# Optimization experiments

Hardware: AMD Instinct MI355X
Metric: run time of the kernel (lower is better)

The kernel has to match this reference:

```python
import jax, jax.numpy as jnp
import numpy as np

N_NODES = 100_000
N_EDGES = 1_200_000


def _lap_weights(src, dst, attr, n):
    # PyG get_laplacian(sym) + ChebConv scaling with lambda_max=2.0:
    # L_hat = (2/lmax)(I - D^-1/2 A D^-1/2) - I = -D^-1/2 A D^-1/2 (zero diagonal)
    deg = jnp.zeros((n,), attr.dtype).at[src].add(attr)
    dis = jnp.where(deg > 0, jax.lax.rsqrt(jnp.maximum(deg, 1e-30)), 0.0)
    return -(dis[src] * attr * dis[dst])


def _prop(x, src, dst, lw, n):
    # y_i = sum_{(j->i)} lw_e * x_j   (gather -> scale -> scatter-add)
    return jnp.zeros((n, x.shape[1]), x.dtype).at[dst].add(lw[:, None] * x[src])


def _cheb(x, src, dst, lw, W, b):
    # W: [K, F_in, F_out]; Tx0 = x, Tx1 = L_hat x (K<=2 here)
    out = x @ W[0]
    if W.shape[0] > 1:
        tx1 = _prop(x, src, dst, lw, x.shape[0])
        out = out + tx1 @ W[1]
    return out + b


def setup_inputs() -> dict:
    key = jax.random.key(0)
    ks = jax.random.split(key, 11)
    x = jax.random.normal(ks[0], (N_NODES, 20), jnp.float32)
    edge_index = jax.random.randint(ks[1], (2, N_EDGES), 0, N_NODES, jnp.int32)
    attr = jax.random.uniform(ks[2], (N_EDGES,), jnp.float32)
    def glorot(k, shape):
        fan = shape[-2] + shape[-1]
        return jax.random.normal(k, shape, jnp.float32) * jnp.sqrt(2.0 / fan)
    return {
        "x": x, "edge_index": edge_index, "attr": attr,
        "w1": glorot(ks[3], (1, 20, 32)), "b1": jnp.zeros((32,), jnp.float32),
        "w2": glorot(ks[4], (2, 32, 64)), "b2": jnp.zeros((64,), jnp.float32),
        "w3": glorot(ks[5], (2, 64, 2)), "b3": jnp.zeros((2,), jnp.float32),
        "gate_w": glorot(ks[6], (2, 1)), "gate_b": jnp.zeros((1,), jnp.float32),
    }


def reference(x, edge_index, attr, w1, b1, w2, b2, w3, b3, gate_w, gate_b):
    n = x.shape[0]
    src, dst = edge_index[0], edge_index[1]
    lw = _lap_weights(src, dst, attr, n)
    h = jax.nn.leaky_relu(_cheb(x, src, dst, lw, w1, b1))   # [N, 32]
    h = jax.nn.leaky_relu(_cheb(h, src, dst, lw, w2, b2))   # [N, 64]
    h = _cheb(h, src, dst, lw, w3, b3)                       # [N, 2]
    # GlobalAttention with batch = zeros (single graph): softmax over nodes
    gate = jax.nn.softmax(h @ gate_w + gate_b, axis=0)       # [N, 1]
    pooled = jnp.sum(gate * h, axis=0, keepdims=True)        # [1, 2]
    return jax.nn.log_softmax(pooled, axis=1)
```

## Files before the change

### kernel.cpp

```cpp
#include <hip/hip_runtime.h>
#include <hip/hip_bf16.h>
#include <math.h>

#define N_NODES 100000
#define N_EDGES 1200000
#define E4 (N_EDGES / 4)
#define G2B ((N_NODES + 255) / 256)
#define NB_L1 G2B
#define RANGE 12800
#define NRANGE 8
#define CHK 32
#define NB_DEG (NRANGE * CHK)
#define GPC ((E4 + CHK - 1) / CHK)
#define NBIN 391
#define BINCAP 3584
#define NB_P1 256
#define GP1 ((E4 + NB_P1 - 1) / NB_P1)
#define WQ (8.f * 32767.f)

__device__ __forceinline__ float disf(float d) {
    return (d > 0.f) ? rsqrtf(d) : 0.f;
}

__global__ void degbin_kernel(const int4* __restrict__ src4, const float4* __restrict__ attr4,
                              float* __restrict__ partial) {
    __shared__ float ldeg[RANGE];
    int rb = blockIdx.x;
    int r = rb / CHK;
    int c = rb - r * CHK;
    int base = r * RANGE;
    for (int j = threadIdx.x; j < RANGE; j += blockDim.x) ldeg[j] = 0.f;
    __syncthreads();
    int g0 = c * GPC;
    int g1 = g0 + GPC; if (g1 > E4) g1 = E4;
    for (int g = g0 + threadIdx.x; g < g1; g += blockDim.x) {
        int4 s = src4[g];
        float4 a = attr4[g];
        unsigned o;
        o = (unsigned)(s.x - base); if (o < RANGE) atomicAdd(&ldeg[o], a.x);
        o = (unsigned)(s.y - base); if (o < RANGE) atomicAdd(&ldeg[o], a.y);
        o = (unsigned)(s.z - base); if (o < RANGE) atomicAdd(&ldeg[o], a.z);
        o = (unsigned)(s.w - base); if (o < RANGE) atomicAdd(&ldeg[o], a.w);
    }
    __syncthreads();
    float* dstp = partial + (size_t)rb * RANGE;
    for (int j = threadIdx.x; j < RANGE; j += blockDim.x) dstp[j] = ldeg[j];
}

__global__ void degred_kernel(const float* __restrict__ partial, float* __restrict__ deg) {
    int i = blockIdx.x * blockDim.x + threadIdx.x;
    if (i >= N_NODES) return;
    int r = i / RANGE;
    int j = i - r * RANGE;
    const float* p = partial + (size_t)r * CHK * RANGE + j;
    float s = 0.f;
#pragma unroll
    for (int c = 0; c < CHK; c++) s += p[(size_t)c * RANGE];
    deg[i] = s;
}

__global__ void p1l1_kernel(const int4* __restrict__ src4, const int4* __restrict__ dst4,
                            const float4* __restrict__ attr4, const float* __restrict__ deg,
                            const float* __restrict__ x, const float* __restrict__ w1,
                            const float* __restrict__ b1,
                            int* __restrict__ binCursor, uint2* __restrict__ binRegion,
                            signed char* __restrict__ h1q, float* __restrict__ sscale) {
    __shared__ int lhist[NBIN];
    __shared__ int lbase[NBIN];
    __shared__ int lcnt[NBIN];
    __shared__ float sw[20 * 32];
    __shared__ float sb[32];

    if (blockIdx.x < NB_P1) {
        int g0 = blockIdx.x * GP1;
        int g1 = g0 + GP1; if (g1 > E4) g1 = E4;
        for (int j = threadIdx.x; j < NBIN; j += blockDim.x) { lhist[j] = 0; lcnt[j] = 0; }
        __syncthreads();
        for (int g = g0 + threadIdx.x; g < g1; g += blockDim.x) {
            int4 d = dst4[g];
            atomicAdd(&lhist[d.x >> 8], 1);
            atomicAdd(&lhist[d.y >> 8], 1);
            atomicAdd(&lhist[d.z >> 8], 1);
            atomicAdd(&lhist[d.w >> 8], 1);
        }
        __syncthreads();
        for (int j = threadIdx.x; j < NBIN; j += blockDim.x)
            lbase[j] = (lhist[j] > 0) ? atomicAdd(&binCursor[j], lhist[j]) : 0;
        __syncthreads();
        for (int g = g0 + threadIdx.x; g < g1; g += blockDim.x) {
            int4 s = src4[g];
            int4 d = dst4[g];
            float4 a = attr4[g];
            {
                int bin = d.x >> 8;
                float w = a.x * disf(deg[s.x]);
                int pos = lbase[bin] + atomicAdd(&lcnt[bin], 1);
                if (pos < BINCAP)
                    binRegion[(size_t)bin * BINCAP + pos] =
                        make_uint2(((unsigned)s.x << 8) | (unsigned)(d.x & 255), __float_as_uint(w));
            }
            {
                int bin = d.y >> 8;
                float w = a.y * disf(deg[s.y]);
                int pos = lbase[bin] + atomicAdd(&lcnt[bin], 1);
                if (pos < BINCAP)
                    binRegion[(size_t)bin * BINCAP + pos] =
                        make_uint2(((unsigned)s.y << 8) | (unsigned)(d.y & 255), __float_as_uint(w));
            }
            {
                int bin = d.z >> 8;
                float w = a.z * disf(deg[s.z]);
                int pos = lbase[bin] + atomicAdd(&lcnt[bin], 1);
                if (pos < BINCAP)
                    binRegion[(size_t)bin * BINCAP + pos] =
                        make_uint2(((unsigned)s.z << 8) | (unsigned)(d.z & 255), __float_as_uint(w));
            }
            {
                int bin = d.w >> 8;
                float w = a.w * disf(deg[s.w]);
                int pos = lbase[bin] + atomicAdd(&lcnt[bin], 1);
                if (pos < BINCAP)
                    binRegion[(size_t)bin * BINCAP + pos] =
                        make_uint2(((unsigned)s.w << 8) | (unsigned)(d.w & 255), __float_as_uint(w));
            }
        }
    } else {
        for (int t = threadIdx.x; t < 20 * 32; t += blockDim.x) sw[t] = w1[t];
        if (threadIdx.x < 32) sb[threadIdx.x] = b1[threadIdx.x];
        __syncthreads();
        int i = (blockIdx.x - NB_P1) * blockDim.x + threadIdx.x;
        if (i >= N_NODES) return;
        float xr[20];
#pragma unroll
        for (int k = 0; k < 20; k++) xr[k] = x[(size_t)i * 20 + k];
        float row[32];
        float rmax = 0.f;
#pragma unroll
        for (int j = 0; j < 32; j++) {
            float a = sb[j];
#pragma unroll
            for (int k = 0; k < 20; k++) a += xr[k] * sw[k * 32 + j];
            a = (a > 0.f) ? a : 0.01f * a;
            row[j] = a;
            rmax = fmaxf(rmax, fabsf(a));
        }
        float sc = fmaxf(rmax * (1.f / 127.f), 1e-4f);
        float inv = 1.f / sc;
        sscale[i] = sc;
#pragma unroll
        for (int j = 0; j < 32; j++) {
            h1q[(size_t)i * 32 + j] = (signed char)lrintf(row[j] * inv);
        }
    }
}

__global__ void binscan_kernel(const int* __restrict__ binCursor, int* __restrict__ bin_start) {
    __shared__ int sm[512];
    int t = threadIdx.x;
    int v = 0;
    if (t < NBIN) {
        v = binCursor[t];
        if (v > BINCAP) v = BINCAP;
    }
    sm[t] = v;
    __syncthreads();
    for (int off = 1; off < 512; off <<= 1) {
        int u = (t >= off) ? sm[t - off] : 0;
        __syncthreads();
        sm[t] += u;
        __syncthreads();
    }
    if (t < NBIN) bin_start[t + 1] = sm[t];
    if (t == 0) bin_start[0] = 0;
}

__global__ void p2_kernel(const uint2* __restrict__ binRegion, const int* __restrict__ bin_start,
                          const float* __restrict__ sscale,
                          int* __restrict__ row_start, unsigned* __restrict__ csr) {
    __shared__ uint2 recs[BINCAP];
    __shared__ int hist[256];
    __shared__ int excl[256];
    __shared__ int cnt[256];
    int b = blockIdx.x;
    int t = threadIdx.x;
    int base = bin_start[b];
    int c = bin_start[b + 1] - base;
    const uint2* reg = binRegion + (size_t)b * BINCAP;
    for (int j = t; j < c; j += 256) recs[j] = reg[j];
    hist[t] = 0; cnt[t] = 0;
    __syncthreads();
    for (int j = t; j < c; j += 256) atomicAdd(&hist[recs[j].x & 255u], 1);
    __syncthreads();
    int v = hist[t];
    excl[t] = v;
    __syncthreads();
    for (int off = 1; off < 256; off <<= 1) {
        int u = (t >= off) ? excl[t - off] : 0;
        __syncthreads();
        excl[t] += u;
        __syncthreads();
    }
    int ex = excl[t] - v;
    row_start[b * 256 + t] = base + ex;
    if (b == NBIN - 1 && t == 255) row_start[NBIN * 256] = bin_start[NBIN];
    __syncthreads();
    hist[t] = ex;
    __syncthreads();
    for (int j = t; j < c; j += 256) {
        unsigned w0 = recs[j].x;
        int low = (int)(w0 & 255u);
        int src = (int)(w0 >> 8);
        float w = __uint_as_float(recs[j].y);
        float ws = w * sscale[src] * WQ;
        unsigned q = (unsigned)(ws + 0.5f);
        if (q > 32767u) q = 32767u;
        int pos = hist[low] + atomicAdd(&cnt[low], 1);
        csr[base + pos] = ((unsigned)src << 15) | q;
    }
}

__global__ void gl2_kernel(const int* __restrict__ row_start, const unsigned* __restrict__ csr,
                           const float* __restrict__ deg, const signed char* __restrict__ h1q,
                           const float* __restrict__ sscale,
                           const float* __restrict__ w2, const float* __restrict__ b2,
                           const float* __restrict__ w3,
                           float2* __restrict__ z0, float2* __restrict__ z1w) {
    __shared__ float s0[32 * 64];
    __shared__ float s1[32 * 64];
    __shared__ float sw3[256];
    __shared__ float sb[64];
    __shared__ float h1s[8][32];
    __shared__ float t1s[8][32];
    for (int t = threadIdx.x; t < 32 * 64; t += blockDim.x) {
        s0[t] = w2[t];
        s1[t] = w2[32 * 64 + t];
    }
    for (int t = threadIdx.x; t < 256; t += blockDim.x) sw3[t] = w3[t];
    if (threadIdx.x < 64) sb[threadIdx.x] = b2[threadIdx.x];
    __syncthreads();

    int grp = threadIdx.x >> 5;
    int lane = threadIdx.x & 31;
    int e4 = lane >> 3;
    int fg = lane & 7;
    int node = blockIdx.x * 8 + grp;
    bool alive = (node < N_NODES);

    int acc0 = 0, acc1 = 0, acc2 = 0, acc3 = 0;
    if (alive) {
        int rs = row_start[node], re = row_start[node + 1];
        for (int j = rs + e4; j < re; j += 4) {
            unsigned e = csr[j];
            int sa = (int)(e >> 15);
            int wq = (int)(e & 0x7FFFu);
            int packed = *reinterpret_cast<const int*>(h1q + (size_t)sa * 32 + fg * 4);
            acc0 += wq * (int)(signed char)(packed);
            acc1 += wq * (int)(signed char)(packed >> 8);
            acc2 += wq * (int)(signed char)(packed >> 16);
            acc3 += wq * (int)(signed char)(packed >> 24);
        }
    }
    acc0 += __shfl_xor(acc0, 8);  acc0 += __shfl_xor(acc0, 16);
    acc1 += __shfl_xor(acc1, 8);  acc1 += __shfl_xor(acc1, 16);
    acc2 += __shfl_xor(acc2, 8);  acc2 += __shfl_xor(acc2, 16);
    acc3 += __shfl_xor(acc3, 8);  acc3 += __shfl_xor(acc3, 16);

    if (alive && e4 == 0) {
        float dn = -disf(deg[node]) * (1.f / WQ);
        int packed = *reinterpret_cast<const int*>(h1q + (size_t)node * 32 + fg * 4);
        float sc = sscale[node];
        h1s[grp][fg * 4 + 0] = sc * (float)(signed char)(packed);
        h1s[grp][fg * 4 + 1] = sc * (float)(signed char)(packed >> 8);
        h1s[grp][fg * 4 + 2] = sc * (float)(signed char)(packed >> 16);
        h1s[grp][fg * 4 + 3] = sc * (float)(signed char)(packed >> 24);
        t1s[grp][fg * 4 + 0] = dn * (float)acc0;
        t1s[grp][fg * 4 + 1] = dn * (float)acc1;
        t1s[grp][fg * 4 + 2] = dn * (float)acc2;
        t1s[grp][fg * 4 + 3] = dn * (float)acc3;
    }
    __syncthreads();

    int f = lane;
    float a0 = sb[f], a1 = sb[f + 32];
#pragma unroll 8
    for (int k = 0; k < 32; k++) {
        float h = h1s[grp][k];
        float tv = t1s[grp][k];
        a0 += h * s0[k * 64 + f]      + tv * s1[k * 64 + f];
        a1 += h * s0[k * 64 + f + 32] + tv * s1[k * 64 + f + 32];
    }
    float v0 = (a0 > 0.f) ? a0 : 0.01f * a0;
    float v1 = (a1 > 0.f) ? a1 : 0.01f * a1;

    float z00 = v0 * sw3[f * 2 + 0] + v1 * sw3[(f + 32) * 2 + 0];
    float z01 = v0 * sw3[f * 2 + 1] + v1 * sw3[(f + 32) * 2 + 1];
    float z10 = v0 * sw3[128 + f * 2 + 0] + v1 * sw3[128 + (f + 32) * 2 + 0];
    float z11 = v0 * sw3[128 + f * 2 + 1] + v1 * sw3[128 + (f + 32) * 2 + 1];
#pragma unroll
    for (int m = 16; m > 0; m >>= 1) {
        z00 += __shfl_xor(z00, m);
        z01 += __shfl_xor(z01, m);
        z10 += __shfl_xor(z10, m);
        z11 += __shfl_xor(z11, m);
    }
    if (alive && f == 0) {
        z0[node] = make_float2(z00, z01);
        float isc = 1.f / sscale[node];
        z1w[node] = make_float2(z10 * isc, z11 * isc);
    }
}

__global__ void g2acc_kernel(const int* __restrict__ row_start, const unsigned* __restrict__ csr,
                             const float* __restrict__ deg,
                             const float2* __restrict__ z0, const float2* __restrict__ z1w,
                             const float* __restrict__ b3, const float* __restrict__ gw,
                             const float* __restrict__ gb, float4* __restrict__ quads) {
    __shared__ float sm[256], ss[256], s0[256], s1[256];
    int t = threadIdx.x;
    int i = blockIdx.x * blockDim.x + t;
    float m = -INFINITY, se = 0.f, a0 = 0.f, a1 = 0.f;
    if (i < N_NODES) {
        int rs = row_start[i], re = row_start[i + 1];
        float acc0 = 0.f, acc1 = 0.f;
        for (int j = rs; j < re; j++) {
            unsigned e = csr[j];
            int s = (int)(e >> 15);
            float wq = (float)(e & 0x7FFFu);
            float2 zv = z1w[s];
            acc0 += wq * zv.x;
            acc1 += wq * zv.y;
        }
        float di = -disf(deg[i]) * (1.f / WQ);
        float2 z0v = z0[i];
        float o0 = z0v.x + di * acc0 + b3[0];
        float o1 = z0v.y + di * acc1 + b3[1];
        m = o0 * gw[0] + o1 * gw[1] + gb[0];
        se = 1.f; a0 = o0; a1 = o1;
    }
    sm[t] = m; ss[t] = se; s0[t] = a0; s1[t] = a1;
    __syncthreads();
    for (int s = 128; s > 0; s >>= 1) {
        if (t < s) {
            float mb = sm[t + s];
            if (mb != -INFINITY) {
                float ma = sm[t];
                if (ma == -INFINITY) {
                    sm[t] = mb; ss[t] = ss[t + s]; s0[t] = s0[t + s]; s1[t] = s1[t + s];
                } else if (mb <= ma) {
                    float c = __expf(mb - ma);
                    ss[t] += ss[t + s] * c;
                    s0[t] += s0[t + s] * c;
                    s1[t] += s1[t + s] * c;
                } else {
                    float c = __expf(ma - mb);
                    ss[t] = ss[t] * c + ss[t + s];
                    s0[t] = s0[t] * c + s0[t + s];
                    s1[t] = s1[t] * c + s1[t + s];
                    sm[t] = mb;
                }
            }
        }
        __syncthreads();
    }
    if (t == 0) quads[blockIdx.x] = make_float4(sm[0], ss[0], s0[0], s1[0]);
}

__global__ void accB_kernel(const float4* __restrict__ quads, float* __restrict__ out) {
    __shared__ float sm[512], ss[512], s0[512], s1[512];
    int t = threadIdx.x;
    float m = -INFINITY, se = 0.f, a0 = 0.f, a1 = 0.f;
    if (t < G2B) {
        float4 q = quads[t];
        m = q.x; se = q.y; a0 = q.z; a1 = q.w;
    }
    sm[t] = m; ss[t] = se; s0[t] = a0; s1[t] = a1;
    __syncthreads();
    for (int s = 256; s > 0; s >>= 1) {
        if (t < s) {
            float mb = sm[t + s];
            if (mb != -INFINITY) {
                float ma = sm[t];
                if (ma == -INFINITY) {
                    sm[t] = mb; ss[t] = ss[t + s]; s0[t] = s0[t + s]; s1[t] = s1[t + s];
                } else if (mb <= ma) {
                    float c = __expf(mb - ma);
                    ss[t] += ss[t + s] * c;
                    s0[t] += s0[t + s] * c;
                    s1[t] += s1[t + s] * c;
                } else {
                    float c = __expf(ma - mb);
                    ss[t] = ss[t] * c + ss[t + s];
                    s0[t] = s0[t] * c + s0[t + s];
                    s1[t] = s1[t] * c + s1[t + s];
                    sm[t] = mb;
                }
            }
        }
        __syncthreads();
    }
    if (t == 0) {
        float se0 = ss[0];
        float p0 = s0[0] / se0;
        float p1 = s1[0] / se0;
        float mm = fmaxf(p0, p1);
        float l = mm + logf(__expf(p0 - mm) + __expf(p1 - mm));
        out[0] = p0 - l;
        out[1] = p1 - l;
    }
}

extern "C" void kernel_launch(void* const* d_in, const int* in_sizes, int n_in,
                              void* d_out, int out_size, void* d_ws, size_t ws_size,
                              hipStream_t stream) {
    const float* x    = (const float*)d_in[0];
    const int*   ei   = (const int*)d_in[1];
    const float* attr = (const float*)d_in[2];
    const float* w1   = (const float*)d_in[3];
    const float* b1   = (const float*)d_in[4];
    const float* w2   = (const float*)d_in[5];
    const float* b2   = (const float*)d_in[6];
    const float* w3   = (const float*)d_in[7];
    const float* b3   = (const float*)d_in[8];
    const float* gw   = (const float*)d_in[9];
    const float* gb   = (const float*)d_in[10];
    float* out = (float*)d_out;

    const int4*   src4  = (const int4*)ei;
    const int4*   dst4  = (const int4*)(ei + N_EDGES);
    const float4* attr4 = (const float4*)attr;

    float* ws = (float*)d_ws;
    size_t off = 0;
    int*      binCursor = (int*)(ws + off); off += NBIN;
    int*      bin_start = (int*)(ws + off); off += NBIN + 1;
    float*    deg       = ws + off; off += N_NODES;
    float*    sscale    = ws + off; off += N_NODES;
    int*      row_start = (int*)(ws + off); off += NBIN * 256 + 1;
    float*    partial   = ws + off; off += (size_t)NB_DEG * RANGE;
    off = (off + 3) & ~(size_t)3;
    uint2*    binRegion = (uint2*)(ws + off); off += (size_t)NBIN * BINCAP * 2;
    unsigned* csr       = (unsigned*)(ws + off); off += N_EDGES;
    signed char* h1q    = (signed char*)(ws + off); off += (size_t)N_NODES * 8;
    float2*   z0  = (float2*)(ws + off); off += (size_t)N_NODES * 2;
    float2*   z1w = (float2*)(ws + off); off += (size_t)N_NODES * 2;
    off = (off + 3) & ~(size_t)3;
    float4*   quads = (float4*)(ws + off); off += (size_t)G2B * 4;

    const int B = 256;
    auto cdiv = [](long long a, long long b) { return (int)((a + b - 1) / b); };

    hipMemsetAsync(binCursor, 0, NBIN * sizeof(int), stream);

    degbin_kernel<<<NB_DEG, B, 0, stream>>>(src4, attr4, partial);
    degred_kernel<<<cdiv(N_NODES, B), B, 0, stream>>>(partial, deg);

    p1l1_kernel<<<NB_P1 + NB_L1, B, 0, stream>>>(src4, dst4, attr4, deg, x, w1, b1,
                                                 binCursor, binRegion, h1q, sscale);

    binscan_kernel<<<1, 512, 0, stream>>>(binCursor, bin_start);

    p2_kernel<<<NBIN, B, 0, stream>>>(binRegion, bin_start, sscale, row_start, csr);

    gl2_kernel<<<cdiv(N_NODES, 8), B, 0, stream>>>(row_start, csr, deg, h1q, sscale,
                                                   w2, b2, w3, z0, z1w);

    g2acc_kernel<<<G2B, B, 0, stream>>>(row_start, csr, deg, z0, z1w, b3, gw, gb, quads);

    accB_kernel<<<1, 512, 0, stream>>>(quads, out);
}
```

Before: 162.4 us.

## Restructure gl2 to one 64-lane wave per node and amortize weight loads

Result: slower. 244.3 us (+50.4%).

```diff
diff --git a/kernel.cpp b/kernel.cpp
--- a/kernel.cpp
+++ b/kernel.cpp
@@ -9,14 +9,16 @@
 #define NB_L1 G2B
 #define RANGE 12800
 #define NRANGE 8
-#define CHK 32
+#define CHK 64
 #define NB_DEG (NRANGE * CHK)
 #define GPC ((E4 + CHK - 1) / CHK)
 #define NBIN 391
 #define BINCAP 3584
-#define NB_P1 256
+#define NB_P1 512
 #define GP1 ((E4 + NB_P1 - 1) / NB_P1)
 #define WQ (8.f * 32767.f)
+#define GL2_NPB 64
+#define NB_GL2 ((N_NODES + GL2_NPB - 1) / GL2_NPB)
 
 __device__ __forceinline__ float disf(float d) {
     return (d > 0.f) ? rsqrtf(d) : 0.f;
@@ -229,84 +231,88 @@
     __shared__ float s1[32 * 64];
     __shared__ float sw3[256];
     __shared__ float sb[64];
-    __shared__ float h1s[8][32];
-    __shared__ float t1s[8][32];
-    for (int t = threadIdx.x; t < 32 * 64; t += blockDim.x) {
-        s0[t] = w2[t];
-        s1[t] = w2[32 * 64 + t];
-    }
-    for (int t = threadIdx.x; t < 256; t += blockDim.x) sw3[t] = w3[t];
-    if (threadIdx.x < 64) sb[threadIdx.x] = b2[threadIdx.x];
-    __syncthreads();
-
-    int grp = threadIdx.x >> 5;
-    int lane = threadIdx.x & 31;
-    int e4 = lane >> 3;
+    int tid = threadIdx.x;
+    for (int t = tid; t < 32 * 64; t += 512) { s0[t] = w2[t]; s1[t] = w2[2048 + t]; }
+    for (int t = tid; t < 256; t += 512) sw3[t] = w3[t];
+    if (tid < 64) sb[tid] = b2[tid];
+    __syncthreads();
+
+    int wave = tid >> 6;
+    int lane = tid & 63;
     int fg = lane & 7;
-    int node = blockIdx.x * 8 + grp;
-    bool alive = (node < N_NODES);
-
-    int acc0 = 0, acc1 = 0, acc2 = 0, acc3 = 0;
-    if (alive) {
-        int rs = row_start[node], re = row_start[node + 1];
-        for (int j = rs + e4; j < re; j += 4) {
-            unsigned e = csr[j];
-            int sa = (int)(e >> 15);
-            int wq = (int)(e & 0x7FFFu);
-            int packed = *reinterpret_cast<const int*>(h1q + (size_t)sa * 32 + fg * 4);
-            acc0 += wq * (int)(signed char)(packed);
-            acc1 += wq * (int)(signed char)(packed >> 8);
-            acc2 += wq * (int)(signed char)(packed >> 16);
-            acc3 += wq * (int)(signed char)(packed >> 24);
-        }
-    }
-    acc0 += __shfl_xor(acc0, 8);  acc0 += __shfl_xor(acc0, 16);
-    acc1 += __shfl_xor(acc1, 8);  acc1 += __shfl_xor(acc1, 16);
-    acc2 += __shfl_xor(acc2, 8);  acc2 += __shfl_xor(acc2, 16);
-    acc3 += __shfl_xor(acc3, 8);  acc3 += __shfl_xor(acc3, 16);
-
-    if (alive && e4 == 0) {
-        float dn = -disf(deg[node]) * (1.f / WQ);
-        int packed = *reinterpret_cast<const int*>(h1q + (size_t)node * 32 + fg * 4);
-        float sc = sscale[node];
-        h1s[grp][fg * 4 + 0] = sc * (float)(signed char)(packed);
-        h1s[grp][fg * 4 + 1] = sc * (float)(signed char)(packed >> 8);
-        h1s[grp][fg * 4 + 2] = sc * (float)(signed char)(packed >> 16);
-        h1s[grp][fg * 4 + 3] = sc * (float)(signed char)(packed >> 24);
-        t1s[grp][fg * 4 + 0] = dn * (float)acc0;
-        t1s[grp][fg * 4 + 1] = dn * (float)acc1;
-        t1s[grp][fg * 4 + 2] = dn * (float)acc2;
-        t1s[grp][fg * 4 + 3] = dn * (float)acc3;
-    }
-    __syncthreads();
-
-    int f = lane;
-    float a0 = sb[f], a1 = sb[f + 32];
-#pragma unroll 8
-    for (int k = 0; k < 32; k++) {
-        float h = h1s[grp][k];
-        float tv = t1s[grp][k];
-        a0 += h * s0[k * 64 + f]      + tv * s1[k * 64 + f];
-        a1 += h * s0[k * 64 + f + 32] + tv * s1[k * 64 + f + 32];
-    }
-    float v0 = (a0 > 0.f) ? a0 : 0.01f * a0;
-    float v1 = (a1 > 0.f) ? a1 : 0.01f * a1;
-
-    float z00 = v0 * sw3[f * 2 + 0] + v1 * sw3[(f + 32) * 2 + 0];
-    float z01 = v0 * sw3[f * 2 + 1] + v1 * sw3[(f + 32) * 2 + 1];
-    float z10 = v0 * sw3[128 + f * 2 + 0] + v1 * sw3[128 + (f + 32) * 2 + 0];
-    float z11 = v0 * sw3[128 + f * 2 + 1] + v1 * sw3[128 + (f + 32) * 2 + 1];
-#pragma unroll
-    for (int m = 16; m > 0; m >>= 1) {
-        z00 += __shfl_xor(z00, m);
-        z01 += __shfl_xor(z01, m);
-        z10 += __shfl_xor(z10, m);
-        z11 += __shfl_xor(z11, m);
-    }
-    if (alive && f == 0) {
-        z0[node] = make_float2(z00, z01);
-        float isc = 1.f / sscale[node];
-        z1w[node] = make_float2(z10 * isc, z11 * isc);
+    int e8 = lane >> 3;
+
+    for (int round = 0; round < GL2_NPB / 8; ++round) {
+        int node = blockIdx.x * GL2_NPB + round * 8 + wave;
+        bool alive = (node < N_NODES);
+
+        int acc0 = 0, acc1 = 0, acc2 = 0, acc3 = 0;
+        if (alive) {
+            int rs = row_start[node], re = row_start[node + 1];
+            for (int j = rs + e8; j < re; j += 8) {
+                unsigned e = csr[j];
+                int sa = (int)(e >> 15);
+                int wq = (int)(e & 0x7FFFu);
+                int packed = *reinterpret_cast<const int*>(h1q + (size_t)sa * 32 + fg * 4);
+                acc0 += wq * (int)(signed char)(packed);
+                acc1 += wq * (int)(signed char)(packed >> 8);
+                acc2 += wq * (int)(signed char)(packed >> 16);
+                acc3 += wq * (int)(signed char)(packed >> 24);
+            }
+        }
+        acc0 += __shfl_xor(acc0, 8);  acc0 += __shfl_xor(acc0, 16);  acc0 += __shfl_xor(acc0, 32);
+        acc1 += __shfl_xor(acc1, 8);  acc1 += __shfl_xor(acc1, 16);  acc1 += __shfl_xor(acc1, 32);
+        acc2 += __shfl_xor(acc2, 8);  acc2 += __shfl_xor(acc2, 16);  acc2 += __shfl_xor(acc2, 32);
+        acc3 += __shfl_xor(acc3, 8);  acc3 += __shfl_xor(acc3, 16);  acc3 += __shfl_xor(acc3, 32);
+
+        float hr0 = 0.f, hr1 = 0.f, hr2 = 0.f, hr3 = 0.f;
+        float tr0 = 0.f, tr1 = 0.f, tr2 = 0.f, tr3 = 0.f;
+        float isc = 1.f;
+        if (alive) {
+            int packed = *reinterpret_cast<const int*>(h1q + (size_t)node * 32 + fg * 4);
+            float sc = sscale[node];
+            isc = 1.f / sc;
+            float dn = -disf(deg[node]) * (1.f / WQ);
+            hr0 = sc * (float)(signed char)(packed);
+            hr1 = sc * (float)(signed char)(packed >> 8);
+            hr2 = sc * (float)(signed char)(packed >> 16);
+            hr3 = sc * (float)(signed char)(packed >> 24);
+            tr0 = dn * (float)acc0;
+            tr1 = dn * (float)acc1;
+            tr2 = dn * (float)acc2;
+            tr3 = dn * (float)acc3;
+        }
+
+        float a = sb[lane];
+#pragma unroll
+        for (int k = 0; k < 32; ++k) {
+            const int q = k >> 2;
+            float hv, tv;
+            switch (k & 3) {
+                case 0: hv = __shfl(hr0, q); tv = __shfl(tr0, q); break;
+                case 1: hv = __shfl(hr1, q); tv = __shfl(tr1, q); break;
+                case 2: hv = __shfl(hr2, q); tv = __shfl(tr2, q); break;
+                default: hv = __shfl(hr3, q); tv = __shfl(tr3, q); break;
+            }
+            a += hv * s0[k * 64 + lane] + tv * s1[k * 64 + lane];
+        }
+        float v = (a > 0.f) ? a : 0.01f * a;
+
+        float z00 = v * sw3[lane * 2 + 0];
+        float z01 = v * sw3[lane * 2 + 1];
+        float z10 = v * sw3[128 + lane * 2 + 0];
+        float z11 = v * sw3[128 + lane * 2 + 1];
+#pragma unroll
+        for (int m = 32; m > 0; m >>= 1) {
+            z00 += __shfl_xor(z00, m);
+            z01 += __shfl_xor(z01, m);
+            z10 += __shfl_xor(z10, m);
+            z11 += __shfl_xor(z11, m);
+        }
+        if (alive && lane == 0) {
+            z0[node] = make_float2(z00, z01);
+            z1w[node] = make_float2(z10 * isc, z11 * isc);
+        }
     }
 }
 
@@ -461,8 +467,8 @@
 
     p2_kernel<<<NBIN, B, 0, stream>>>(binRegion, bin_start, sscale, row_start, csr);
 
-    gl2_kernel<<<cdiv(N_NODES, 8), B, 0, stream>>>(row_start, csr, deg, h1q, sscale,
-                                                   w2, b2, w3, z0, z1w);
+    gl2_kernel<<<NB_GL2, 512, 0, stream>>>(row_start, csr, deg, h1q, sscale,
+                                           w2, b2, w3, z0, z1w);
 
     g2acc_kernel<<<G2B, B, 0, stream>>>(row_start, csr, deg, z0, z1w, b3, gw, gb, quads);
 
```
